# Kernel optimization log

Hardware: AMD Instinct MI355X
Metric: run time of the kernel (lower is better)

## Reference

```python
import jax, jax.numpy as jnp
import numpy as np

N_NODES = 25000
N_EDGES = 250000
IN_DIM = 256
HID = 128
HEADS = 2
NEG_SLOPE_ATT = 0.2   # PyG GATConv default negative_slope
NEG_SLOPE_ACT = 0.01  # F.leaky_relu default


def setup_inputs() -> dict:
    key = jax.random.key(0)
    ks = jax.random.split(key, 8)
    x = jax.random.normal(ks[0], (N_NODES, IN_DIM), dtype=jnp.float32)
    edge_index = jax.random.randint(ks[1], (2, N_EDGES), 0, N_NODES, dtype=jnp.int32)
    # GATConv params: lin weight [heads*out, in], att vectors [heads, out], bias [heads*out]
    s = 1.0 / np.sqrt(IN_DIM)
    W = jax.random.uniform(ks[2], (HEADS * HID, IN_DIM), jnp.float32, -s, s)
    att_src = jax.random.uniform(ks[3], (HEADS, HID), jnp.float32, -s, s)
    att_dst = jax.random.uniform(ks[4], (HEADS, HID), jnp.float32, -s, s)
    bias = jnp.zeros((HEADS * HID,), jnp.float32)
    s2 = 1.0 / np.sqrt(HEADS * HID * 2)
    fc1_w = jax.random.uniform(ks[5], (3, HEADS * HID * 2), jnp.float32, -s2, s2)
    fc1_b = jax.random.uniform(ks[6], (3,), jnp.float32, -s2, s2)
    return {"x": x, "edge_index": edge_index, "W": W, "att_src": att_src,
            "att_dst": att_dst, "bias": bias, "fc1_w": fc1_w, "fc1_b": fc1_b}


def _gat_conv(x, edge_index, W, att_src, att_dst, bias):
    N = x.shape[0]
    h = (x @ W.T).reshape(N, HEADS, HID)             # [N,H,C]
    a_src = jnp.einsum('nhc,hc->nh', h, att_src)     # [N,H]
    a_dst = jnp.einsum('nhc,hc->nh', h, att_dst)
    # add self loops (PyG GATConv default)
    loops = jnp.arange(N, dtype=edge_index.dtype)
    src = jnp.concatenate([edge_index[0], loops])
    dst = jnp.concatenate([edge_index[1], loops])
    e = jax.nn.leaky_relu(a_src[src] + a_dst[dst], NEG_SLOPE_ATT)  # [E+N,H]
    # scatter-softmax over destination nodes
    m = jax.ops.segment_max(e, dst, num_segments=N)
    ex = jnp.exp(e - m[dst])
    z = jax.ops.segment_sum(ex, dst, num_segments=N)
    alpha = ex / z[dst]                              # [E+N,H]
    msg = alpha[:, :, None] * h[src]                 # [E+N,H,C]
    out = jax.ops.segment_sum(msg, dst, num_segments=N)  # [N,H,C]
    return out.reshape(N, HEADS * HID) + bias


def reference(x, edge_index, W, att_src, att_dst, bias, fc1_w, fc1_b):
    # dropout is identity in eval mode
    h = _gat_conv(x, edge_index, W, att_src, att_dst, bias)
    h = jax.nn.leaky_relu(h, NEG_SLOPE_ACT)
    edge_rep = jnp.concatenate([h[edge_index[0]], h[edge_index[1]]], axis=1)  # [E, 4*HID]
    return edge_rep @ fc1_w.T + fc1_b               # [E, 3]
```

## Files before the change

kernel.cpp:

```cpp
#include <hip/hip_runtime.h>
#include <hip/hip_bf16.h>

#define N_NODES 25000
#define N_EDGES 250000
#define N_TOT   275000
#define FDIM    256
#define M_PAD   25024
#define MAXDEG  64

typedef __attribute__((ext_vector_type(8))) short bf16x8;
typedef __attribute__((ext_vector_type(4))) float f32x4;

__device__ inline float bf2f(unsigned short s) {
    union { unsigned u; float f; } v; v.u = ((unsigned)s) << 16;
    return v.f;
}

__global__ __launch_bounds__(512) void k_gemm(const float* __restrict__ x,
                                              const float* __restrict__ W,
                                              const float* __restrict__ att_src,
                                              const float* __restrict__ att_dst,
                                              __hip_bfloat16* __restrict__ hb,
                                              float* __restrict__ a_src,
                                              float* __restrict__ a_dst) {
    __shared__ char lds[40960];
    __shared__ float s_as[64][2];
    __shared__ float s_ad[64][2];
    const int m0   = blockIdx.x * 64;
    const int t    = threadIdx.x;
    const int lane = t & 63;
    const int wid  = t >> 6;
    const int wr   = wid >> 2;
    const int wc   = wid & 3;

    if (t < 256) {
        s_as[t >> 2][t & 1] = 0.f;
        s_ad[t >> 2][t & 1] = 0.f;
    }
    f32x4 acc[2][4];
    #pragma unroll
    for (int mi = 0; mi < 2; ++mi)
        #pragma unroll
        for (int ni = 0; ni < 4; ++ni)
            acc[mi][ni] = (f32x4){0.f, 0.f, 0.f, 0.f};

    for (int kc = 0; kc < 256; kc += 64) {
        __syncthreads();
        #pragma unroll
        for (int q = 0; q < 2; ++q) {
            int fi = q * 512 + t;
            int row = fi >> 4, ks4 = fi & 15;
            int node = m0 + row;
            f32x4 v = (f32x4){0.f, 0.f, 0.f, 0.f};
            if (node < N_NODES) v = *reinterpret_cast<const f32x4*>(x + node * 256 + kc + ks4 * 4);
            __hip_bfloat16 b[4];
            b[0] = __float2bfloat16(v.x); b[1] = __float2bfloat16(v.y);
            b[2] = __float2bfloat16(v.z); b[3] = __float2bfloat16(v.w);
            int byte = (row * 128 + ks4 * 8) ^ ((row & 7) << 4);
            *reinterpret_cast<ushort4*>(lds + byte) = *reinterpret_cast<const ushort4*>(b);
        }
        #pragma unroll
        for (int q = 0; q < 8; ++q) {
            int fi = q * 512 + t;
            int col = fi >> 4, ks4 = fi & 15;
            f32x4 v = *reinterpret_cast<const f32x4*>(W + col * 256 + kc + ks4 * 4);
            __hip_bfloat16 b[4];
            b[0] = __float2bfloat16(v.x); b[1] = __float2bfloat16(v.y);
            b[2] = __float2bfloat16(v.z); b[3] = __float2bfloat16(v.w);
            int byte = 8192 + ((col * 128 + ks4 * 8) ^ ((col & 7) << 4));
            *reinterpret_cast<ushort4*>(lds + byte) = *reinterpret_cast<const ushort4*>(b);
        }
        __syncthreads();
        #pragma unroll
        for (int ks = 0; ks < 2; ++ks) {
            bf16x8 a[2], b[4];
            #pragma unroll
            for (int mi = 0; mi < 2; ++mi) {
                int row = wr * 32 + mi * 16 + (lane & 15);
                int byte = (row * 128 + ks * 64 + (lane >> 4) * 16) ^ ((row & 7) << 4);
                a[mi] = *reinterpret_cast<const bf16x8*>(lds + byte);
            }
            #pragma unroll
            for (int ni = 0; ni < 4; ++ni) {
                int col = wc * 64 + ni * 16 + (lane & 15);
                int byte = 8192 + ((col * 128 + ks * 64 + (lane >> 4) * 16) ^ ((col & 7) << 4));
                b[ni] = *reinterpret_cast<const bf16x8*>(lds + byte);
            }
            #pragma unroll
            for (int mi = 0; mi < 2; ++mi)
                #pragma unroll
                for (int ni = 0; ni < 4; ++ni)
                    acc[mi][ni] = __builtin_amdgcn_mfma_f32_16x16x32_bf16(
                        a[mi], b[ni], acc[mi][ni], 0, 0, 0);
        }
    }
    #pragma unroll
    for (int mi = 0; mi < 2; ++mi)
        #pragma unroll
        for (int r = 0; r < 4; ++r) {
            int row = m0 + wr * 32 + mi * 16 + (lane >> 4) * 4 + r;
            #pragma unroll
            for (int ni = 0; ni < 4; ++ni) {
                int col = wc * 64 + ni * 16 + (lane & 15);
                hb[row * 256 + col] = __float2bfloat16(acc[mi][ni][r]);
            }
        }
    const int hd0 = wc >> 1;
    float as_[4], ad_[4];
    #pragma unroll
    for (int ni = 0; ni < 4; ++ni) {
        int col = wc * 64 + ni * 16 + (lane & 15);
        as_[ni] = att_src[col];
        ad_[ni] = att_dst[col];
    }
    #pragma unroll
    for (int mi = 0; mi < 2; ++mi)
        #pragma unroll
        for (int r = 0; r < 4; ++r) {
            float ps = acc[mi][0][r] * as_[0] + acc[mi][1][r] * as_[1]
                     + acc[mi][2][r] * as_[2] + acc[mi][3][r] * as_[3];
            float pd = acc[mi][0][r] * ad_[0] + acc[mi][1][r] * ad_[1]
                     + acc[mi][2][r] * ad_[2] + acc[mi][3][r] * ad_[3];
            #pragma unroll
            for (int o = 8; o > 0; o >>= 1) {
                ps += __shfl_down(ps, o);
                pd += __shfl_down(pd, o);
            }
            if ((lane & 15) == 0) {
                int rl = wr * 32 + mi * 16 + (lane >> 4) * 4 + r;
                atomicAdd(&s_as[rl][hd0], ps);
                atomicAdd(&s_ad[rl][hd0], pd);
            }
        }
    __syncthreads();
    if (t < 128) {
        int rl = t >> 1, hd = t & 1;
        int row = m0 + rl;
        if (row < N_NODES) {
            a_src[row * 2 + hd] = s_as[rl][hd];
            a_dst[row * 2 + hd] = s_ad[rl][hd];
        }
    }
}

__global__ void k_csr_fill(const int* __restrict__ ei,
                           const float* __restrict__ a_src,
                           const float* __restrict__ a_dst,
                           int* __restrict__ cnt,
                           float4* __restrict__ csr) {
    int i = blockIdx.x * 256 + threadIdx.x;
    if (i >= N_TOT) return;
    int src, dst;
    if (i < N_EDGES) { src = ei[i]; dst = ei[N_EDGES + i]; }
    else             { src = dst = i - N_EDGES; }
    float2 as = *reinterpret_cast<const float2*>(a_src + src * 2);
    float2 ad = *reinterpret_cast<const float2*>(a_dst + dst * 2);
    float v0 = as.x + ad.x;
    float v1 = as.y + ad.y;
    v0 = v0 > 0.f ? v0 : 0.2f * v0;
    v1 = v1 > 0.f ? v1 : 0.2f * v1;
    int pos = dst * MAXDEG + atomicAdd(&cnt[dst], 1);
    float4 r;
    r.x = __int_as_float(src);
    r.y = expf(v0);
    r.z = expf(v1);
    r.w = 0.f;
    csr[pos] = r;
}

__global__ __launch_bounds__(256) void k_node_aggregate(const float4* __restrict__ csr,
                                                        const int* __restrict__ cnt,
                                                        const unsigned short* __restrict__ hb,
                                                        const float* __restrict__ bias,
                                                        const float* __restrict__ fc1_w,
                                                        const float* __restrict__ fc1_b,
                                                        float* __restrict__ p_src,
                                                        float* __restrict__ p_dst) {
    const int n = (blockIdx.x << 2) + (threadIdx.x >> 6);
    const int lane = threadIdx.x & 63;
    if (n >= N_NODES) return;
    const int s = n * MAXDEG;
    const int e = s + cnt[n];
    f32x4 acc0 = (f32x4){0.f, 0.f, 0.f, 0.f};
    f32x4 acc1 = (f32x4){0.f, 0.f, 0.f, 0.f};
    f32x4 acc2 = (f32x4){0.f, 0.f, 0.f, 0.f};
    f32x4 acc3 = (f32x4){0.f, 0.f, 0.f, 0.f};
    float zs0 = 0.f, zs1 = 0.f, zs2 = 0.f, zs3 = 0.f;
    int it = s;
    for (; it + 4 <= e; it += 4) {
        float4 r0 = csr[it], r1 = csr[it + 1], r2 = csr[it + 2], r3 = csr[it + 3];
        int s0 = __float_as_int(r0.x), s1 = __float_as_int(r1.x);
        int s2 = __float_as_int(r2.x), s3 = __float_as_int(r3.x);
        float w0 = lane < 32 ? r0.y : r0.z;
        float w1 = lane < 32 ? r1.y : r1.z;
        float w2 = lane < 32 ? r2.y : r2.z;
        float w3 = lane < 32 ? r3.y : r3.z;
        ushort4 h0 = *reinterpret_cast<const ushort4*>(hb + s0 * FDIM + lane * 4);
        ushort4 h1 = *reinterpret_cast<const ushort4*>(hb + s1 * FDIM + lane * 4);
        ushort4 h2 = *reinterpret_cast<const ushort4*>(hb + s2 * FDIM + lane * 4);
        ushort4 h3 = *reinterpret_cast<const ushort4*>(hb + s3 * FDIM + lane * 4);
        acc0.x += w0 * bf2f(h0.x); acc0.y += w0 * bf2f(h0.y);
        acc0.z += w0 * bf2f(h0.z); acc0.w += w0 * bf2f(h0.w);
        acc1.x += w1 * bf2f(h1.x); acc1.y += w1 * bf2f(h1.y);
        acc1.z += w1 * bf2f(h1.z); acc1.w += w1 * bf2f(h1.w);
        acc2.x += w2 * bf2f(h2.x); acc2.y += w2 * bf2f(h2.y);
        acc2.z += w2 * bf2f(h2.z); acc2.w += w2 * bf2f(h2.w);
        acc3.x += w3 * bf2f(h3.x); acc3.y += w3 * bf2f(h3.y);
        acc3.z += w3 * bf2f(h3.z); acc3.w += w3 * bf2f(h3.w);
        zs0 += w0; zs1 += w1; zs2 += w2; zs3 += w3;
    }
    for (; it < e; ++it) {
        float4 r0 = csr[it];
        int s0 = __float_as_int(r0.x);
        float w0 = lane < 32 ? r0.y : r0.z;
        ushort4 h0 = *reinterpret_cast<const ushort4*>(hb + s0 * FDIM + lane * 4);
        acc0.x += w0 * bf2f(h0.x); acc0.y += w0 * bf2f(h0.y);
        acc0.z += w0 * bf2f(h0.z); acc0.w += w0 * bf2f(h0.w);
        zs0 += w0;
    }
    const float inv = 1.f / ((zs0 + zs1) + (zs2 + zs3));
    f32x4 bv = *reinterpret_cast<const f32x4*>(bias + lane * 4);
    float h2_0 = ((acc0.x + acc1.x) + (acc2.x + acc3.x)) * inv + bv.x;
    float h2_1 = ((acc0.y + acc1.y) + (acc2.y + acc3.y)) * inv + bv.y;
    float h2_2 = ((acc0.z + acc1.z) + (acc2.z + acc3.z)) * inv + bv.z;
    float h2_3 = ((acc0.w + acc1.w) + (acc2.w + acc3.w)) * inv + bv.w;
    h2_0 = h2_0 > 0.f ? h2_0 : 0.01f * h2_0;
    h2_1 = h2_1 > 0.f ? h2_1 : 0.01f * h2_1;
    h2_2 = h2_2 > 0.f ? h2_2 : 0.01f * h2_2;
    h2_3 = h2_3 > 0.f ? h2_3 : 0.01f * h2_3;
    f32x4 wa0 = *reinterpret_cast<const f32x4*>(fc1_w + 0 * 512 + lane * 4);
    f32x4 wa1 = *reinterpret_cast<const f32x4*>(fc1_w + 1 * 512 + lane * 4);
    f32x4 wa2 = *reinterpret_cast<const f32x4*>(fc1_w + 2 * 512 + lane * 4);
    f32x4 wb0 = *reinterpret_cast<const f32x4*>(fc1_w + 0 * 512 + 256 + lane * 4);
    f32x4 wb1 = *reinterpret_cast<const f32x4*>(fc1_w + 1 * 512 + 256 + lane * 4);
    f32x4 wb2 = *reinterpret_cast<const f32x4*>(fc1_w + 2 * 512 + 256 + lane * 4);
    float v0 = wa0.x * h2_0 + wa0.y * h2_1 + wa0.z * h2_2 + wa0.w * h2_3;
    float v1 = wa1.x * h2_0 + wa1.y * h2_1 + wa1.z * h2_2 + wa1.w * h2_3;
    float v2 = wa2.x * h2_0 + wa2.y * h2_1 + wa2.z * h2_2 + wa2.w * h2_3;
    float v3 = wb0.x * h2_0 + wb0.y * h2_1 + wb0.z * h2_2 + wb0.w * h2_3;
    float v4 = wb1.x * h2_0 + wb1.y * h2_1 + wb1.z * h2_2 + wb1.w * h2_3;
    float v5 = wb2.x * h2_0 + wb2.y * h2_1 + wb2.z * h2_2 + wb2.w * h2_3;
    #pragma unroll
    for (int o = 32; o > 0; o >>= 1) {
        v0 += __shfl_down(v0, o); v1 += __shfl_down(v1, o); v2 += __shfl_down(v2, o);
        v3 += __shfl_down(v3, o); v4 += __shfl_down(v4, o); v5 += __shfl_down(v5, o);
    }
    if (lane == 0) {
        f32x4 ps = (f32x4){v0 + fc1_b[0], v1 + fc1_b[1], v2 + fc1_b[2], 0.f};
        f32x4 pd = (f32x4){v3, v4, v5, 0.f};
        *reinterpret_cast<f32x4*>(p_src + n * 4) = ps;
        *reinterpret_cast<f32x4*>(p_dst + n * 4) = pd;
    }
}

__global__ void k_edge_out(const int* __restrict__ ei,
                           const float* __restrict__ p_src,
                           const float* __restrict__ p_dst,
                           float* __restrict__ out) {
    int i0 = (blockIdx.x * 256 + threadIdx.x) * 4;
    if (i0 >= N_EDGES) return;
    int4 sv = *reinterpret_cast<const int4*>(ei + i0);
    int4 dv = *reinterpret_cast<const int4*>(ei + N_EDGES + i0);
    f32x4 p0 = *reinterpret_cast<const f32x4*>(p_src + sv.x * 4);
    f32x4 p1 = *reinterpret_cast<const f32x4*>(p_src + sv.y * 4);
    f32x4 p2 = *reinterpret_cast<const f32x4*>(p_src + sv.z * 4);
    f32x4 p3 = *reinterpret_cast<const f32x4*>(p_src + sv.w * 4);
    f32x4 q0 = *reinterpret_cast<const f32x4*>(p_dst + dv.x * 4);
    f32x4 q1 = *reinterpret_cast<const f32x4*>(p_dst + dv.y * 4);
    f32x4 q2 = *reinterpret_cast<const f32x4*>(p_dst + dv.z * 4);
    f32x4 q3 = *reinterpret_cast<const f32x4*>(p_dst + dv.w * 4);
    f32x4 o0 = (f32x4){p0.x + q0.x, p0.y + q0.y, p0.z + q0.z, p1.x + q1.x};
    f32x4 o1 = (f32x4){p1.y + q1.y, p1.z + q1.z, p2.x + q2.x, p2.y + q2.y};
    f32x4 o2 = (f32x4){p2.z + q2.z, p3.x + q3.x, p3.y + q3.y, p3.z + q3.z};
    f32x4* op = reinterpret_cast<f32x4*>(out + i0 * 3);
    op[0] = o0; op[1] = o1; op[2] = o2;
}

extern "C" void kernel_launch(void* const* d_in, const int* in_sizes, int n_in,
                              void* d_out, int out_size, void* d_ws, size_t ws_size,
                              hipStream_t stream) {
    const float* x       = (const float*)d_in[0];
    const int*   ei      = (const int*)d_in[1];
    const float* W       = (const float*)d_in[2];
    const float* att_src = (const float*)d_in[3];
    const float* att_dst = (const float*)d_in[4];
    const float* bias    = (const float*)d_in[5];
    const float* fc1_w   = (const float*)d_in[6];
    const float* fc1_b   = (const float*)d_in[7];
    float* out = (float*)d_out;

    float4* csr = (float4*)d_ws;
    __hip_bfloat16* hb = (__hip_bfloat16*)(csr + N_NODES * MAXDEG);
    float* a_src = (float*)(hb + M_PAD * FDIM);
    float* a_dst = a_src + 2 * N_NODES;
    float* p_src = a_dst + 2 * N_NODES;
    float* p_dst = p_src + 4 * N_NODES;
    int* cnt     = (int*)(p_dst + 4 * N_NODES);

    hipMemsetAsync(cnt, 0, N_NODES * sizeof(int), stream);
    k_gemm<<<(M_PAD / 64), 512, 0, stream>>>(x, W, att_src, att_dst, hb, a_src, a_dst);
    k_csr_fill<<<(N_TOT + 255) / 256, 256, 0, stream>>>(ei, a_src, a_dst, cnt, csr);
    k_node_aggregate<<<(N_NODES + 3) / 4, 256, 0, stream>>>(
        csr, cnt, (const unsigned short*)hb, bias, fc1_w, fc1_b, p_src, p_dst);
    k_edge_out<<<(N_EDGES / 4 + 255) / 256, 256, 0, stream>>>(ei, p_src, p_dst, out);
}
```

Measured before the change: 145.3 us.

## Aggregate two nodes per wavefront with 16-byte gathers, fold count reset into GEMM

The node aggregation kernel now gives each node half a wavefront (32 lanes) instead of a full 64, and each lane loads 8 bf16 values with one 16-byte load instead of 4. The tail loop is replaced by a clamped, masked 4-wide loop, and the final reduction uses 32-wide shuffles. The hipMemsetAsync that zeroed the per-node counters is removed, and the GEMM kernel now zeroes them, saving one launch. The aim is fewer, wider gather instructions and better lane use for low-degree nodes. The cost is more register pressure per lane and some wasted loads on the padded tail entries.

```diff
diff --git a/kernel.cpp b/kernel.cpp
--- a/kernel.cpp
+++ b/kernel.cpp
@@ -10,6 +10,7 @@
 
 typedef __attribute__((ext_vector_type(8))) short bf16x8;
 typedef __attribute__((ext_vector_type(4))) float f32x4;
+typedef __attribute__((ext_vector_type(8))) unsigned short u16x8;
 
 __device__ inline float bf2f(unsigned short s) {
     union { unsigned u; float f; } v; v.u = ((unsigned)s) << 16;
@@ -22,7 +23,8 @@
                                               const float* __restrict__ att_dst,
                                               __hip_bfloat16* __restrict__ hb,
                                               float* __restrict__ a_src,
-                                              float* __restrict__ a_dst) {
+                                              float* __restrict__ a_dst,
+                                              int* __restrict__ cnt) {
     __shared__ char lds[40960];
     __shared__ float s_as[64][2];
     __shared__ float s_ad[64][2];
@@ -32,6 +34,9 @@
     const int wid  = t >> 6;
     const int wr   = wid >> 2;
     const int wc   = wid & 3;
+
+    int gid = blockIdx.x * 512 + t;
+    if (gid < N_NODES) cnt[gid] = 0;
 
     if (t < 256) {
         s_as[t >> 2][t & 1] = 0.f;
@@ -176,78 +181,81 @@
                                                         const float* __restrict__ fc1_b,
                                                         float* __restrict__ p_src,
                                                         float* __restrict__ p_dst) {
-    const int n = (blockIdx.x << 2) + (threadIdx.x >> 6);
     const int lane = threadIdx.x & 63;
+    const int half = lane >> 5;
+    const int l    = lane & 31;
+    const int n = (blockIdx.x << 3) + ((threadIdx.x >> 6) << 1) + half;
     if (n >= N_NODES) return;
+    const int hd = l >> 4;
     const int s = n * MAXDEG;
     const int e = s + cnt[n];
-    f32x4 acc0 = (f32x4){0.f, 0.f, 0.f, 0.f};
-    f32x4 acc1 = (f32x4){0.f, 0.f, 0.f, 0.f};
-    f32x4 acc2 = (f32x4){0.f, 0.f, 0.f, 0.f};
-    f32x4 acc3 = (f32x4){0.f, 0.f, 0.f, 0.f};
-    float zs0 = 0.f, zs1 = 0.f, zs2 = 0.f, zs3 = 0.f;
-    int it = s;
-    for (; it + 4 <= e; it += 4) {
-        float4 r0 = csr[it], r1 = csr[it + 1], r2 = csr[it + 2], r3 = csr[it + 3];
-        int s0 = __float_as_int(r0.x), s1 = __float_as_int(r1.x);
-        int s2 = __float_as_int(r2.x), s3 = __float_as_int(r3.x);
-        float w0 = lane < 32 ? r0.y : r0.z;
-        float w1 = lane < 32 ? r1.y : r1.z;
-        float w2 = lane < 32 ? r2.y : r2.z;
-        float w3 = lane < 32 ? r3.y : r3.z;
-        ushort4 h0 = *reinterpret_cast<const ushort4*>(hb + s0 * FDIM + lane * 4);
-        ushort4 h1 = *reinterpret_cast<const ushort4*>(hb + s1 * FDIM + lane * 4);
-        ushort4 h2 = *reinterpret_cast<const ushort4*>(hb + s2 * FDIM + lane * 4);
-        ushort4 h3 = *reinterpret_cast<const ushort4*>(hb + s3 * FDIM + lane * 4);
-        acc0.x += w0 * bf2f(h0.x); acc0.y += w0 * bf2f(h0.y);
-        acc0.z += w0 * bf2f(h0.z); acc0.w += w0 * bf2f(h0.w);
-        acc1.x += w1 * bf2f(h1.x); acc1.y += w1 * bf2f(h1.y);
-        acc1.z += w1 * bf2f(h1.z); acc1.w += w1 * bf2f(h1.w);
-        acc2.x += w2 * bf2f(h2.x); acc2.y += w2 * bf2f(h2.y);
-        acc2.z += w2 * bf2f(h2.z); acc2.w += w2 * bf2f(h2.w);
-        acc3.x += w3 * bf2f(h3.x); acc3.y += w3 * bf2f(h3.y);
-        acc3.z += w3 * bf2f(h3.z); acc3.w += w3 * bf2f(h3.w);
-        zs0 += w0; zs1 += w1; zs2 += w2; zs3 += w3;
-    }
-    for (; it < e; ++it) {
-        float4 r0 = csr[it];
-        int s0 = __float_as_int(r0.x);
-        float w0 = lane < 32 ? r0.y : r0.z;
-        ushort4 h0 = *reinterpret_cast<const ushort4*>(hb + s0 * FDIM + lane * 4);
-        acc0.x += w0 * bf2f(h0.x); acc0.y += w0 * bf2f(h0.y);
-        acc0.z += w0 * bf2f(h0.z); acc0.w += w0 * bf2f(h0.w);
-        zs0 += w0;
-    }
-    const float inv = 1.f / ((zs0 + zs1) + (zs2 + zs3));
-    f32x4 bv = *reinterpret_cast<const f32x4*>(bias + lane * 4);
-    float h2_0 = ((acc0.x + acc1.x) + (acc2.x + acc3.x)) * inv + bv.x;
-    float h2_1 = ((acc0.y + acc1.y) + (acc2.y + acc3.y)) * inv + bv.y;
-    float h2_2 = ((acc0.z + acc1.z) + (acc2.z + acc3.z)) * inv + bv.z;
-    float h2_3 = ((acc0.w + acc1.w) + (acc2.w + acc3.w)) * inv + bv.w;
-    h2_0 = h2_0 > 0.f ? h2_0 : 0.01f * h2_0;
-    h2_1 = h2_1 > 0.f ? h2_1 : 0.01f * h2_1;
-    h2_2 = h2_2 > 0.f ? h2_2 : 0.01f * h2_2;
-    h2_3 = h2_3 > 0.f ? h2_3 : 0.01f * h2_3;
-    f32x4 wa0 = *reinterpret_cast<const f32x4*>(fc1_w + 0 * 512 + lane * 4);
-    f32x4 wa1 = *reinterpret_cast<const f32x4*>(fc1_w + 1 * 512 + lane * 4);
-    f32x4 wa2 = *reinterpret_cast<const f32x4*>(fc1_w + 2 * 512 + lane * 4);
-    f32x4 wb0 = *reinterpret_cast<const f32x4*>(fc1_w + 0 * 512 + 256 + lane * 4);
-    f32x4 wb1 = *reinterpret_cast<const f32x4*>(fc1_w + 1 * 512 + 256 + lane * 4);
-    f32x4 wb2 = *reinterpret_cast<const f32x4*>(fc1_w + 2 * 512 + 256 + lane * 4);
-    float v0 = wa0.x * h2_0 + wa0.y * h2_1 + wa0.z * h2_2 + wa0.w * h2_3;
-    float v1 = wa1.x * h2_0 + wa1.y * h2_1 + wa1.z * h2_2 + wa1.w * h2_3;
-    float v2 = wa2.x * h2_0 + wa2.y * h2_1 + wa2.z * h2_2 + wa2.w * h2_3;
-    float v3 = wb0.x * h2_0 + wb0.y * h2_1 + wb0.z * h2_2 + wb0.w * h2_3;
-    float v4 = wb1.x * h2_0 + wb1.y * h2_1 + wb1.z * h2_2 + wb1.w * h2_3;
-    float v5 = wb2.x * h2_0 + wb2.y * h2_1 + wb2.z * h2_2 + wb2.w * h2_3;
-    #pragma unroll
-    for (int o = 32; o > 0; o >>= 1) {
-        v0 += __shfl_down(v0, o); v1 += __shfl_down(v1, o); v2 += __shfl_down(v2, o);
-        v3 += __shfl_down(v3, o); v4 += __shfl_down(v4, o); v5 += __shfl_down(v5, o);
-    }
-    if (lane == 0) {
-        f32x4 ps = (f32x4){v0 + fc1_b[0], v1 + fc1_b[1], v2 + fc1_b[2], 0.f};
-        f32x4 pd = (f32x4){v3, v4, v5, 0.f};
+    f32x4 accL = (f32x4){0.f, 0.f, 0.f, 0.f};
+    f32x4 accH = (f32x4){0.f, 0.f, 0.f, 0.f};
+    float zs = 0.f;
+    for (int j = s; j < e; j += 4) {
+        int j1 = j + 1 < e ? j + 1 : e - 1;
+        int j2 = j + 2 < e ? j + 2 : e - 1;
+        int j3 = j + 3 < e ? j + 3 : e - 1;
+        float4 r0 = csr[j], r1 = csr[j1], r2 = csr[j2], r3 = csr[j3];
+        float w0 = hd ? r0.z : r0.y;
+        float w1 = hd ? r1.z : r1.y;
+        float w2 = hd ? r2.z : r2.y;
+        float w3 = hd ? r3.z : r3.y;
+        w1 = (j + 1 < e) ? w1 : 0.f;
+        w2 = (j + 2 < e) ? w2 : 0.f;
+        w3 = (j + 3 < e) ? w3 : 0.f;
+        u16x8 h0 = *reinterpret_cast<const u16x8*>(hb + __float_as_int(r0.x) * FDIM + l * 8);
+        u16x8 h1 = *reinterpret_cast<const u16x8*>(hb + __float_as_int(r1.x) * FDIM + l * 8);
+        u16x8 h2 = *reinterpret_cast<const u16x8*>(hb + __float_as_int(r2.x) * FDIM + l * 8);
+        u16x8 h3 = *reinterpret_cast<const u16x8*>(hb + __float_as_int(r3.x) * FDIM + l * 8);
+        accL.x += w0 * bf2f(h0[0]); accL.y += w0 * bf2f(h0[1]);
+        accL.z += w0 * bf2f(h0[2]); accL.w += w0 * bf2f(h0[3]);
+        accH.x += w0 * bf2f(h0[4]); accH.y += w0 * bf2f(h0[5]);
+        accH.z += w0 * bf2f(h0[6]); accH.w += w0 * bf2f(h0[7]);
+        accL.x += w1 * bf2f(h1[0]); accL.y += w1 * bf2f(h1[1]);
+        accL.z += w1 * bf2f(h1[2]); accL.w += w1 * bf2f(h1[3]);
+        accH.x += w1 * bf2f(h1[4]); accH.y += w1 * bf2f(h1[5]);
+        accH.z += w1 * bf2f(h1[6]); accH.w += w1 * bf2f(h1[7]);
+        accL.x += w2 * bf2f(h2[0]); accL.y += w2 * bf2f(h2[1]);
+        accL.z += w2 * bf2f(h2[2]); accL.w += w2 * bf2f(h2[3]);
+        accH.x += w2 * bf2f(h2[4]); accH.y += w2 * bf2f(h2[5]);
+        accH.z += w2 * bf2f(h2[6]); accH.w += w2 * bf2f(h2[7]);
+        accL.x += w3 * bf2f(h3[0]); accL.y += w3 * bf2f(h3[1]);
+        accL.z += w3 * bf2f(h3[2]); accL.w += w3 * bf2f(h3[3]);
+        accH.x += w3 * bf2f(h3[4]); accH.y += w3 * bf2f(h3[5]);
+        accH.z += w3 * bf2f(h3[6]); accH.w += w3 * bf2f(h3[7]);
+        zs += ((w0 + w1) + (w2 + w3));
+    }
+    const float inv = 1.f / zs;
+    f32x4 bL = *reinterpret_cast<const f32x4*>(bias + l * 8);
+    f32x4 bH = *reinterpret_cast<const f32x4*>(bias + l * 8 + 4);
+    float h2v[8];
+    h2v[0] = accL.x * inv + bL.x; h2v[1] = accL.y * inv + bL.y;
+    h2v[2] = accL.z * inv + bL.z; h2v[3] = accL.w * inv + bL.w;
+    h2v[4] = accH.x * inv + bH.x; h2v[5] = accH.y * inv + bH.y;
+    h2v[6] = accH.z * inv + bH.z; h2v[7] = accH.w * inv + bH.w;
+    #pragma unroll
+    for (int d = 0; d < 8; ++d) h2v[d] = h2v[d] > 0.f ? h2v[d] : 0.01f * h2v[d];
+    float v[6];
+    #pragma unroll
+    for (int k = 0; k < 3; ++k) {
+        f32x4 wL = *reinterpret_cast<const f32x4*>(fc1_w + k * 512 + l * 8);
+        f32x4 wH = *reinterpret_cast<const f32x4*>(fc1_w + k * 512 + l * 8 + 4);
+        v[k] = wL.x * h2v[0] + wL.y * h2v[1] + wL.z * h2v[2] + wL.w * h2v[3]
+             + wH.x * h2v[4] + wH.y * h2v[5] + wH.z * h2v[6] + wH.w * h2v[7];
+        f32x4 uL = *reinterpret_cast<const f32x4*>(fc1_w + k * 512 + 256 + l * 8);
+        f32x4 uH = *reinterpret_cast<const f32x4*>(fc1_w + k * 512 + 256 + l * 8 + 4);
+        v[3 + k] = uL.x * h2v[0] + uL.y * h2v[1] + uL.z * h2v[2] + uL.w * h2v[3]
+                 + uH.x * h2v[4] + uH.y * h2v[5] + uH.z * h2v[6] + uH.w * h2v[7];
+    }
+    #pragma unroll
+    for (int o = 16; o > 0; o >>= 1) {
+        #pragma unroll
+        for (int k = 0; k < 6; ++k) v[k] += __shfl_down(v[k], o, 32);
+    }
+    if (l == 0) {
+        f32x4 ps = (f32x4){v[0] + fc1_b[0], v[1] + fc1_b[1], v[2] + fc1_b[2], 0.f};
+        f32x4 pd = (f32x4){v[3], v[4], v[5], 0.f};
         *reinterpret_cast<f32x4*>(p_src + n * 4) = ps;
         *reinterpret_cast<f32x4*>(p_dst + n * 4) = pd;
     }
@@ -297,10 +305,10 @@
     float* p_dst = p_src + 4 * N_NODES;
     int* cnt     = (int*)(p_dst + 4 * N_NODES);
 
-    hipMemsetAsync(cnt, 0, N_NODES * sizeof(int), stream);
-    k_gemm<<<(M_PAD / 64), 512, 0, stream>>>(x, W, att_src, att_dst, hb, a_src, a_dst);
+    k_gemm<<<(M_PAD / 64), 512, 0, stream>>>(x, W, att_src, att_dst, hb,
+                                             a_src, a_dst, cnt);
     k_csr_fill<<<(N_TOT + 255) / 256, 256, 0, stream>>>(ei, a_src, a_dst, cnt, csr);
-    k_node_aggregate<<<(N_NODES + 3) / 4, 256, 0, stream>>>(
+    k_node_aggregate<<<(N_NODES / 8), 256, 0, stream>>>(
         csr, cnt, (const unsigned short*)hb, bias, fc1_w, fc1_b, p_src, p_dst);
     k_edge_out<<<(N_EDGES / 4 + 255) / 256, 256, 0, stream>>>(ei, p_src, p_dst, out);
 }
```

New measurement: 138.1 us. -5.0%, faster.
